# Performance work log

Measured on AMD Instinct MI355X. Metric: run time of the kernel, lower is better.

The kernel has to match this reference:

```python
import jax, jax.numpy as jnp
import numpy as np

Z_CELL = 0.1
Z_HID = 0.1
H = 512


def setup_inputs() -> dict:
    key = jax.random.key(0)
    ks = jax.random.split(key, 5)
    T, B, I = 1024, 32, 512
    s_ih = 1.0 / np.sqrt(I)
    s_hh = 1.0 / np.sqrt(H)
    return {
        "inputs": jax.random.normal(ks[0], (T, B, I), jnp.float32),
        "W_ih": jax.random.normal(ks[1], (4 * H, I), jnp.float32) * s_ih,
        "W_hh": jax.random.normal(ks[2], (4 * H, H), jnp.float32) * s_hh,
        "b_ih": jax.random.normal(ks[3], (4 * H,), jnp.float32) * s_ih,
        "b_hh": jax.random.normal(ks[4], (4 * H,), jnp.float32) * s_hh,
    }


def _run_direction(xw, W_hh, b_hh, batch):
    # xw: [T, B, 4H] precomputed input projection (x @ W_ih.T + b_ih)
    h0 = jnp.zeros((batch, H), xw.dtype)
    c0 = jnp.zeros((batch, H), xw.dtype)

    def step(carry, xw_t):
        h, c = carry
        gates = xw_t + h @ W_hh.T + b_hh  # [B, 4H]
        i, f, g, o = jnp.split(gates, 4, axis=-1)
        i = jax.nn.sigmoid(i)
        f = jax.nn.sigmoid(f)
        g = jnp.tanh(g)
        o = jax.nn.sigmoid(o)
        c_new = f * c + i * g
        h_new = o * jnp.tanh(c_new)
        # zoneout (eval-mode deterministic blend)
        c = (1.0 - Z_CELL) * c_new + Z_CELL * c
        h = (1.0 - Z_HID) * h_new + Z_HID * h
        return (h, c), h

    _, hs = jax.lax.scan(step, (h0, c0), xw)
    return hs  # [T, B, H]


def reference(inputs, W_ih, W_hh, b_ih, b_hh):
    T, B, _ = inputs.shape
    xw = jnp.einsum('tbi,gi->tbg', inputs, W_ih) + b_ih  # [T, B, 4H]
    out_fwd = _run_direction(xw, W_hh, b_hh, B)
    out_bwd = _run_direction(xw[::-1], W_hh, b_hh, B)[::-1]
    return out_fwd + out_bwd
```

## Files before the change

kernel.cpp:

```cpp
#include <hip/hip_runtime.h>

#define T_STEPS 1024
#define BATCH 32
#define HID 512
#define GATES 2048
#define KDIM 512

typedef __attribute__((ext_vector_type(8))) short short8;
typedef __attribute__((ext_vector_type(4))) float floatx4;

__device__ __forceinline__ unsigned short f2bf(float f) {
  union { float f; unsigned u; } v; v.f = f;
  return (unsigned short)((v.u + 0x7FFFu + ((v.u >> 16) & 1u)) >> 16);
}
__device__ __forceinline__ float fsigmoid(float x) {
  return 1.0f / (1.0f + __expf(-x));
}
__device__ __forceinline__ float ftanh(float x) {
  return 2.0f / (1.0f + __expf(-2.0f * x)) - 1.0f;
}

__global__ void init_kernel(unsigned* __restrict__ hbuf_u) {
  int idx = blockIdx.x * 256 + threadIdx.x;
  __hip_atomic_store(&hbuf_u[idx], 0u, __ATOMIC_RELAXED, __HIP_MEMORY_SCOPE_AGENT);
}

__global__ void merge_kernel(float* __restrict__ out,
                             const float* __restrict__ add, int n4) {
  int i = blockIdx.x * 256 + threadIdx.x;
  int stride = gridDim.x * 256;
  for (; i < n4; i += stride) {
    float4 a = ((const float4*)add)[i];
    float4 o = ((float4*)out)[i];
    o.x += a.x; o.y += a.y; o.z += a.z; o.w += a.w;
    ((float4*)out)[i] = o;
  }
}

__global__ __launch_bounds__(512) void lstm_persist(
    const float* __restrict__ X,
    const float* __restrict__ Wih,
    const float* __restrict__ Whh,
    const float* __restrict__ bih,
    const float* __restrict__ bhh,
    float* __restrict__ out,
    unsigned* __restrict__ hw,
    float* __restrict__ obwd) {
  __shared__ unsigned short xs[32][520];
  __shared__ unsigned short hs[32][520];
  __shared__ float gp[2][32][64];

  const int tid = threadIdx.x;
  const int bid = blockIdx.x;
  const int dir = bid >> 5;
  const int bsl = bid & 31;
  const int u0 = bsl * 16;

  unsigned* hwD = hw + dir * 2 * (BATCH * HID);

  const int w = tid >> 6, lane = tid & 63;
  const int kh = w >> 2;
  const int nt = w & 3;
  const int colx = lane & 15, q = lane >> 4;

  short8 bwh[8], bwx[8];
  {
    const size_t roff = (size_t)(nt * HID + u0 + colx) * KDIM + kh * 256 + q * 8;
    const float* wrh = Whh + roff;
    const float* wrx = Wih + roff;
#pragma unroll
    for (int ks = 0; ks < 8; ++ks) {
      float4 h0 = *(const float4*)(wrh + ks * 32);
      float4 h1 = *(const float4*)(wrh + ks * 32 + 4);
      union { unsigned short u[8]; short8 v; } pk;
      pk.u[0] = f2bf(h0.x); pk.u[1] = f2bf(h0.y); pk.u[2] = f2bf(h0.z); pk.u[3] = f2bf(h0.w);
      pk.u[4] = f2bf(h1.x); pk.u[5] = f2bf(h1.y); pk.u[6] = f2bf(h1.z); pk.u[7] = f2bf(h1.w);
      bwh[ks] = pk.v;
      float4 x0 = *(const float4*)(wrx + ks * 32);
      float4 x1 = *(const float4*)(wrx + ks * 32 + 4);
      union { unsigned short u[8]; short8 v; } px;
      px.u[0] = f2bf(x0.x); px.u[1] = f2bf(x0.y); px.u[2] = f2bf(x0.z); px.u[3] = f2bf(x0.w);
      px.u[4] = f2bf(x1.x); px.u[5] = f2bf(x1.y); px.u[6] = f2bf(x1.z); px.u[7] = f2bf(x1.w);
      bwx[ks] = px.v;
    }
  }

  const int b = tid >> 4, u = tid & 15;
  const float bias_i = bih[0 * HID + u0 + u] + bhh[0 * HID + u0 + u];
  const float bias_f = bih[1 * HID + u0 + u] + bhh[1 * HID + u0 + u];
  const float bias_g = bih[2 * HID + u0 + u] + bhh[2 * HID + u0 + u];
  const float bias_o = bih[3 * HID + u0 + u] + bhh[3 * HID + u0 + u];

  float c_st = 0.f, h_prev = 0.f;

  float* odst = nullptr;
  if (obwd) odst = dir ? obwd : out;

  float4 xr[8];
  {
    const int t0 = dir ? (T_STEPS - 1) : 0;
    const float* xt = X + (size_t)t0 * BATCH * KDIM;
#pragma unroll
    for (int r = 0; r < 8; ++r) {
      int idx = tid + r * 512;
      xr[r] = *(const float4*)(xt + (size_t)(idx >> 7) * KDIM + (idx & 127) * 4);
    }
  }

  for (int s = 0; s < T_STEPS; ++s) {
    const int t = dir ? (T_STEPS - 1 - s) : s;

#pragma unroll
    for (int r = 0; r < 8; ++r) {
      int idx = tid + r * 512;
      union { unsigned short u[4]; uint2 v; } p;
      p.u[0] = f2bf(xr[r].x); p.u[1] = f2bf(xr[r].y);
      p.u[2] = f2bf(xr[r].z); p.u[3] = f2bf(xr[r].w);
      *(uint2*)&xs[idx >> 7][(idx & 127) * 4] = p.v;
    }
    __syncthreads();

    const unsigned long long* hq =
        (const unsigned long long*)(hwD + (s & 1) * (BATCH * HID));
    const unsigned long long rep = ((unsigned long long)(unsigned)s << 16) |
                                   ((unsigned long long)(unsigned)s << 48);
    const unsigned long long msk = 0xFFFF0000FFFF0000ULL;
    unsigned long long v[16];
#pragma unroll
    for (int r = 0; r < 16; ++r)
      v[r] = __hip_atomic_load(&hq[tid + r * 512], __ATOMIC_RELAXED,
                               __HIP_MEMORY_SCOPE_AGENT);

    floatx4 acc0 = {0.f, 0.f, 0.f, 0.f}, acc1 = {0.f, 0.f, 0.f, 0.f};
    {
      const unsigned short* a0p = &xs[colx][kh * 256 + q * 8];
      const unsigned short* a1p = &xs[16 + colx][kh * 256 + q * 8];
#pragma unroll
      for (int ks = 0; ks < 8; ++ks) {
        short8 a0 = *(const short8*)(a0p + ks * 32);
        short8 a1 = *(const short8*)(a1p + ks * 32);
        acc0 = __builtin_amdgcn_mfma_f32_16x16x32_bf16(a0, bwx[ks], acc0, 0, 0, 0);
        acc1 = __builtin_amdgcn_mfma_f32_16x16x32_bf16(a1, bwx[ks], acc1, 0, 0, 0);
      }
    }

    for (;;) {
      unsigned long long bad = 0;
#pragma unroll
      for (int r = 0; r < 16; ++r) bad |= (v[r] ^ rep);
      if (!(bad & msk)) break;
#pragma unroll
      for (int r = 0; r < 16; ++r)
        v[r] = __hip_atomic_load(&hq[tid + r * 512], __ATOMIC_RELAXED,
                                 __HIP_MEMORY_SCOPE_AGENT);
    }

    {
      const int sn = (s + 1 < T_STEPS) ? (s + 1) : s;
      const int tn = dir ? (T_STEPS - 1 - sn) : sn;
      const float* xt = X + (size_t)tn * BATCH * KDIM;
#pragma unroll
      for (int r = 0; r < 8; ++r) {
        int idx = tid + r * 512;
        xr[r] = *(const float4*)(xt + (size_t)(idx >> 7) * KDIM + (idx & 127) * 4);
      }
    }

#pragma unroll
    for (int r = 0; r < 16; ++r) {
      int g = tid + r * 512;
      unsigned packed = (unsigned)(v[r] & 0xFFFFu) |
                        ((unsigned)(v[r] >> 32) << 16);
      *(unsigned*)&hs[g >> 8][(g & 255) * 2] = packed;
    }
    __syncthreads();

    {
      const unsigned short* a0p = &hs[colx][kh * 256 + q * 8];
      const unsigned short* a1p = &hs[16 + colx][kh * 256 + q * 8];
#pragma unroll
      for (int ks = 0; ks < 8; ++ks) {
        short8 a0 = *(const short8*)(a0p + ks * 32);
        short8 a1 = *(const short8*)(a1p + ks * 32);
        acc0 = __builtin_amdgcn_mfma_f32_16x16x32_bf16(a0, bwh[ks], acc0, 0, 0, 0);
        acc1 = __builtin_amdgcn_mfma_f32_16x16x32_bf16(a1, bwh[ks], acc1, 0, 0, 0);
      }
    }
#pragma unroll
    for (int r = 0; r < 4; ++r) {
      gp[kh][q * 4 + r][nt * 16 + colx] = acc0[r];
      gp[kh][16 + q * 4 + r][nt * 16 + colx] = acc1[r];
    }
    __syncthreads();

    float gi = gp[0][b][u]      + gp[1][b][u]      + bias_i;
    float gf = gp[0][b][16 + u] + gp[1][b][16 + u] + bias_f;
    float gg = gp[0][b][32 + u] + gp[1][b][32 + u] + bias_g;
    float go = gp[0][b][48 + u] + gp[1][b][48 + u] + bias_o;
    float si = fsigmoid(gi);
    float sf = fsigmoid(gf);
    float tg = ftanh(gg);
    float so = fsigmoid(go);
    float c_new = sf * c_st + si * tg;
    float h_new = so * ftanh(c_new);
    c_st = 0.9f * c_new + 0.1f * c_st;
    float h = 0.9f * h_new + 0.1f * h_prev;
    h_prev = h;

    {
      unsigned D = (unsigned)f2bf(h) | ((unsigned)(s + 1) << 16);
      unsigned* hop = hwD + ((s + 1) & 1) * (BATCH * HID);
      __hip_atomic_store(&hop[b * HID + u0 + u], D,
                         __ATOMIC_RELAXED, __HIP_MEMORY_SCOPE_AGENT);
    }

    {
      size_t oidx = (size_t)(t * BATCH + b) * HID + u0 + u;
      if (odst) odst[oidx] = h;
      else atomicAdd(out + oidx, h);
    }
  }
}

extern "C" void kernel_launch(void* const* d_in, const int* in_sizes, int n_in,
                              void* d_out, int out_size, void* d_ws, size_t ws_size,
                              hipStream_t stream) {
  const float* X   = (const float*)d_in[0];
  const float* Wih = (const float*)d_in[1];
  const float* Whh = (const float*)d_in[2];
  const float* bih = (const float*)d_in[3];
  const float* bhh = (const float*)d_in[4];
  float* out = (float*)d_out;

  unsigned* hw = (unsigned*)d_ws;

  const size_t OB_OFF = (size_t)1 << 20;
  const size_t OB_BYTES = (size_t)T_STEPS * BATCH * HID * sizeof(float);

  float* obwd = nullptr;
  if (ws_size >= OB_OFF + OB_BYTES)
    obwd = (float*)((char*)d_ws + OB_OFF);

  if (!obwd)
    hipMemsetAsync(d_out, 0, (size_t)out_size * sizeof(float), stream);

  hipLaunchKernelGGL(init_kernel, dim3(256), dim3(256), 0, stream, hw);
  hipLaunchKernelGGL(lstm_persist, dim3(64), dim3(512), 0, stream,
                     X, Wih, Whh, bih, bhh, out, hw, obwd);
  if (obwd)
    hipLaunchKernelGGL(merge_kernel, dim3(2048), dim3(256), 0, stream,
                       out, obwd, (T_STEPS * BATCH * HID) / 4);
}
```

Baseline: 3.785 ms.

## Remap MFMA tiles so each wave owns full K and gates, dropping LDS reduction

Reassigns the wave work split from K-halves by gate-tiles to batch-halves by unit-groups, with each wave running the full 512-wide K reduction and weight columns interleaved so one MFMA tile holds all four gates of four units. Gate values are regrouped in-register with xor shuffles, which removes the gp shared-memory buffer and one __syncthreads per timestep. The h polling switches to inline-asm dwordx4 loads with sc0 sc1 cache bypass and an explicit vmcnt wait. This doubles the weight registers per thread (16+16 short8), which may pressure occupancy or cause spills.

```diff
diff --git a/kernel.cpp b/kernel.cpp
--- a/kernel.cpp
+++ b/kernel.cpp
@@ -3,11 +3,11 @@
 #define T_STEPS 1024
 #define BATCH 32
 #define HID 512
-#define GATES 2048
 #define KDIM 512
 
 typedef __attribute__((ext_vector_type(8))) short short8;
 typedef __attribute__((ext_vector_type(4))) float floatx4;
+typedef __attribute__((ext_vector_type(4))) int int4v;
 
 __device__ __forceinline__ unsigned short f2bf(float f) {
   union { float f; unsigned u; } v; v.f = f;
@@ -18,6 +18,19 @@
 }
 __device__ __forceinline__ float ftanh(float x) {
   return 2.0f / (1.0f + __expf(-2.0f * x)) - 1.0f;
+}
+__device__ __forceinline__ void waitv0() {
+  asm volatile("s_waitcnt vmcnt(0)" ::: "memory");
+}
+
+__device__ __forceinline__ void issue_burst(const unsigned* base, int tid,
+                                            int4v v[8]) {
+#pragma unroll
+  for (int g = 0; g < 8; ++g) {
+    const unsigned* p = base + 4 * (tid + g * 512);
+    asm volatile("global_load_dwordx4 %0, %1, off sc0 sc1"
+                 : "=&v"(v[g]) : "v"(p) : "memory");
+  }
 }
 
 __global__ void init_kernel(unsigned* __restrict__ hbuf_u) {
@@ -48,7 +61,6 @@
     float* __restrict__ obwd) {
   __shared__ unsigned short xs[32][520];
   __shared__ unsigned short hs[32][520];
-  __shared__ float gp[2][32][64];
 
   const int tid = threadIdx.x;
   const int bid = blockIdx.x;
@@ -59,17 +71,21 @@
   unsigned* hwD = hw + dir * 2 * (BATCH * HID);
 
   const int w = tid >> 6, lane = tid & 63;
-  const int kh = w >> 2;
-  const int nt = w & 3;
+  const int mh = w >> 2;
+  const int ug = w & 3;
   const int colx = lane & 15, q = lane >> 4;
-
-  short8 bwh[8], bwx[8];
+  const int g = colx & 3;
+  const int ul = colx >> 2;
+  const int unit = u0 + ug * 4 + ul;
+  const int b_lane = mh * 16 + q * 4 + g;
+
+  short8 bwh[16], bwx[16];
   {
-    const size_t roff = (size_t)(nt * HID + u0 + colx) * KDIM + kh * 256 + q * 8;
+    const size_t roff = (size_t)(g * HID + unit) * KDIM + q * 8;
     const float* wrh = Whh + roff;
     const float* wrx = Wih + roff;
 #pragma unroll
-    for (int ks = 0; ks < 8; ++ks) {
+    for (int ks = 0; ks < 16; ++ks) {
       float4 h0 = *(const float4*)(wrh + ks * 32);
       float4 h1 = *(const float4*)(wrh + ks * 32 + 4);
       union { unsigned short u[8]; short8 v; } pk;
@@ -85,11 +101,10 @@
     }
   }
 
-  const int b = tid >> 4, u = tid & 15;
-  const float bias_i = bih[0 * HID + u0 + u] + bhh[0 * HID + u0 + u];
-  const float bias_f = bih[1 * HID + u0 + u] + bhh[1 * HID + u0 + u];
-  const float bias_g = bih[2 * HID + u0 + u] + bhh[2 * HID + u0 + u];
-  const float bias_o = bih[3 * HID + u0 + u] + bhh[3 * HID + u0 + u];
+  const float bias0 = bih[0 * HID + unit] + bhh[0 * HID + unit];
+  const float bias1 = bih[1 * HID + unit] + bhh[1 * HID + unit];
+  const float bias2 = bih[2 * HID + unit] + bhh[2 * HID + unit];
+  const float bias3 = bih[3 * HID + unit] + bhh[3 * HID + unit];
 
   float c_st = 0.f, h_prev = 0.f;
 
@@ -120,39 +135,38 @@
     }
     __syncthreads();
 
-    const unsigned long long* hq =
-        (const unsigned long long*)(hwD + (s & 1) * (BATCH * HID));
-    const unsigned long long rep = ((unsigned long long)(unsigned)s << 16) |
-                                   ((unsigned long long)(unsigned)s << 48);
-    const unsigned long long msk = 0xFFFF0000FFFF0000ULL;
-    unsigned long long v[16];
-#pragma unroll
-    for (int r = 0; r < 16; ++r)
-      v[r] = __hip_atomic_load(&hq[tid + r * 512], __ATOMIC_RELAXED,
-                               __HIP_MEMORY_SCOPE_AGENT);
-
-    floatx4 acc0 = {0.f, 0.f, 0.f, 0.f}, acc1 = {0.f, 0.f, 0.f, 0.f};
-    {
-      const unsigned short* a0p = &xs[colx][kh * 256 + q * 8];
-      const unsigned short* a1p = &xs[16 + colx][kh * 256 + q * 8];
-#pragma unroll
-      for (int ks = 0; ks < 8; ++ks) {
-        short8 a0 = *(const short8*)(a0p + ks * 32);
-        short8 a1 = *(const short8*)(a1p + ks * 32);
-        acc0 = __builtin_amdgcn_mfma_f32_16x16x32_bf16(a0, bwx[ks], acc0, 0, 0, 0);
-        acc1 = __builtin_amdgcn_mfma_f32_16x16x32_bf16(a1, bwx[ks], acc1, 0, 0, 0);
-      }
-    }
-
-    for (;;) {
-      unsigned long long bad = 0;
-#pragma unroll
-      for (int r = 0; r < 16; ++r) bad |= (v[r] ^ rep);
-      if (!(bad & msk)) break;
-#pragma unroll
-      for (int r = 0; r < 16; ++r)
-        v[r] = __hip_atomic_load(&hq[tid + r * 512], __ATOMIC_RELAXED,
-                                 __HIP_MEMORY_SCOPE_AGENT);
+    const unsigned* hq = hwD + (s & 1) * (BATCH * HID);
+    int4v v[8];
+    issue_burst(hq, tid, v);
+
+    floatx4 acc = {0.f, 0.f, 0.f, 0.f};
+    {
+      const unsigned short* ap = &xs[mh * 16 + colx][q * 8];
+#pragma unroll
+      for (int ks = 0; ks < 16; ++ks) {
+        short8 a = *(const short8*)(ap + ks * 32);
+        acc = __builtin_amdgcn_mfma_f32_16x16x32_bf16(a, bwx[ks], acc, 0, 0, 0);
+      }
+    }
+
+    waitv0();
+    __builtin_amdgcn_sched_barrier(0);
+    {
+      const unsigned rep = (unsigned)s << 16;
+      for (;;) {
+        unsigned bad = 0;
+#pragma unroll
+        for (int gg = 0; gg < 8; ++gg) {
+          bad |= ((unsigned)v[gg].x ^ rep);
+          bad |= ((unsigned)v[gg].y ^ rep);
+          bad |= ((unsigned)v[gg].z ^ rep);
+          bad |= ((unsigned)v[gg].w ^ rep);
+        }
+        if (!(bad & 0xFFFF0000u)) break;
+        issue_burst(hq, tid, v);
+        waitv0();
+        __builtin_amdgcn_sched_barrier(0);
+      }
     }
 
     {
@@ -167,39 +181,51 @@
     }
 
 #pragma unroll
-    for (int r = 0; r < 16; ++r) {
-      int g = tid + r * 512;
-      unsigned packed = (unsigned)(v[r] & 0xFFFFu) |
-                        ((unsigned)(v[r] >> 32) << 16);
-      *(unsigned*)&hs[g >> 8][(g & 255) * 2] = packed;
+    for (int gg = 0; gg < 8; ++gg) {
+      int c = tid + gg * 512;
+      int row = c >> 7;
+      int col = (c & 127) << 2;
+      uint2 pk;
+      pk.x = ((unsigned)v[gg].x & 0xFFFFu) | ((unsigned)v[gg].y << 16);
+      pk.y = ((unsigned)v[gg].z & 0xFFFFu) | ((unsigned)v[gg].w << 16);
+      *(uint2*)&hs[row][col] = pk;
     }
     __syncthreads();
 
     {
-      const unsigned short* a0p = &hs[colx][kh * 256 + q * 8];
-      const unsigned short* a1p = &hs[16 + colx][kh * 256 + q * 8];
-#pragma unroll
-      for (int ks = 0; ks < 8; ++ks) {
-        short8 a0 = *(const short8*)(a0p + ks * 32);
-        short8 a1 = *(const short8*)(a1p + ks * 32);
-        acc0 = __builtin_amdgcn_mfma_f32_16x16x32_bf16(a0, bwh[ks], acc0, 0, 0, 0);
-        acc1 = __builtin_amdgcn_mfma_f32_16x16x32_bf16(a1, bwh[ks], acc1, 0, 0, 0);
-      }
-    }
-#pragma unroll
-    for (int r = 0; r < 4; ++r) {
-      gp[kh][q * 4 + r][nt * 16 + colx] = acc0[r];
-      gp[kh][16 + q * 4 + r][nt * 16 + colx] = acc1[r];
-    }
-    __syncthreads();
-
-    float gi = gp[0][b][u]      + gp[1][b][u]      + bias_i;
-    float gf = gp[0][b][16 + u] + gp[1][b][16 + u] + bias_f;
-    float gg = gp[0][b][32 + u] + gp[1][b][32 + u] + bias_g;
-    float go = gp[0][b][48 + u] + gp[1][b][48 + u] + bias_o;
+      const unsigned short* ap = &hs[mh * 16 + colx][q * 8];
+#pragma unroll
+      for (int ks = 0; ks < 16; ++ks) {
+        short8 a = *(const short8*)(ap + ks * 32);
+        acc = __builtin_amdgcn_mfma_f32_16x16x32_bf16(a, bwh[ks], acc, 0, 0, 0);
+      }
+    }
+
+    float f0, f1, f2, f3;
+    {
+      float u0s = __shfl_xor(acc[0], 2), u1s = __shfl_xor(acc[1], 2);
+      float u2s = __shfl_xor(acc[2], 2), u3s = __shfl_xor(acc[3], 2);
+      bool hi = (g & 2) != 0;
+      float w0 = hi ? u2s : acc[0];
+      float w1 = hi ? u3s : acc[1];
+      float w2 = hi ? acc[2] : u0s;
+      float w3 = hi ? acc[3] : u1s;
+      float z0 = __shfl_xor(w0, 1), z1 = __shfl_xor(w1, 1);
+      float z2 = __shfl_xor(w2, 1), z3 = __shfl_xor(w3, 1);
+      bool od = (g & 1) != 0;
+      f0 = od ? z1 : w0;
+      f1 = od ? w1 : z0;
+      f2 = od ? z3 : w2;
+      f3 = od ? w3 : z2;
+    }
+
+    float gi = f0 + bias0;
+    float gf = f1 + bias1;
+    float gg2 = f2 + bias2;
+    float go = f3 + bias3;
     float si = fsigmoid(gi);
     float sf = fsigmoid(gf);
-    float tg = ftanh(gg);
+    float tg = ftanh(gg2);
     float so = fsigmoid(go);
     float c_new = sf * c_st + si * tg;
     float h_new = so * ftanh(c_new);
@@ -210,12 +236,12 @@
     {
       unsigned D = (unsigned)f2bf(h) | ((unsigned)(s + 1) << 16);
       unsigned* hop = hwD + ((s + 1) & 1) * (BATCH * HID);
-      __hip_atomic_store(&hop[b * HID + u0 + u], D,
+      __hip_atomic_store(&hop[b_lane * HID + unit], D,
                          __ATOMIC_RELAXED, __HIP_MEMORY_SCOPE_AGENT);
     }
 
     {
-      size_t oidx = (size_t)(t * BATCH + b) * HID + u0 + u;
+      size_t oidx = (size_t)(t * BATCH + b_lane) * HID + unit;
       if (odst) odst[oidx] = h;
       else atomicAdd(out + oidx, h);
     }
```

Result: faster. 3.176 ms (-16.1%).
